# Optimization experiments

Hardware: AMD Instinct MI355X
Metric: run time of the kernel (lower is better)

## Reference

```python
import jax, jax.numpy as jnp
import numpy as np
import itertools

# ---- static config (mirrors args in init_kwargs) ----
BS = 4                        # num_processes
H, W = 480, 640               # frame_height, frame_width
NC = 16                       # num_sem_categories
C = 4 + NC                    # obs channels: RGB + depth + semantics
RES = 5                       # map_resolution (cm per cell)
ZRES = 5
MAP_CM = 4800 // 2            # map_size_cm // global_downscaling
M = MAP_CM // RES             # 480 local-map cells
VR = 100                      # vision_range
FOV = 79.0                    # hfov (deg)
DU = 1                        # du_scale
AGENT_H = 1.55 * 100.0        # camera_height * 100 (cm)
MAXH = int(360 / ZRES)        # 72
MINH = int(-40 / ZRES)        # -8
ZH = MAXH - MINH              # 80 height bins
MAP_THR, EXP_THR, CAT_THR = 1.0, 1.0, 5.0
DEG = 57.29577951308232
MIN_Z = int(5 / ZRES - MINH)                    # 9
MAX_Z = int((AGENT_H + 1 + 50) / ZRES - MINH)   # 49
XCAM = (W - 1.0) / 2.0
ZCAM = (H - 1.0) / 2.0
FOC = (W / 2.0) / np.tan(np.deg2rad(FOV / 2.0))


def _splat_feat_nd(feat, coords, grid_dims):
    # feat: (B,F,N) ; coords: (B,3,N) normalized to [-1,1] ; trilinear scatter-add
    B, Fc, N = feat.shape
    G = grid_dims[0] * grid_dims[1] * grid_dims[2]
    grid_flat = jnp.zeros((B, Fc, G), feat.dtype)
    pos_dim, wts_dim = [], []
    for d in range(3):
        gd = grid_dims[d]
        pos = coords[:, d, :] * (gd / 2.0) + gd / 2.0   # (B,N) voxel-space coord
        fl = jnp.floor(pos)
        pd, wd = [], []
        for ix in (0.0, 1.0):
            pos_ix = fl + ix
            safe = ((pos_ix > 0) & (pos_ix < gd)).astype(feat.dtype)
            wd.append((1.0 - jnp.abs(pos - pos_ix)) * safe)
            pd.append(pos_ix * safe)  # unsafe points dumped at index 0 with weight 0
        pos_dim.append(pd)
        wts_dim.append(wd)
    for ix_d in itertools.product((0, 1), (0, 1), (0, 1)):
        w = wts_dim[0][ix_d[0]] * wts_dim[1][ix_d[1]] * wts_dim[2][ix_d[2]]
        idx = jnp.zeros_like(w)
        for d in range(3):
            idx = idx * grid_dims[d] + pos_dim[d][ix_d[d]]
        idx = idx.astype(jnp.int32)                     # (B,N)
        vals = feat * w[:, None, :]                     # (B,F,N)
        grid_flat = jax.vmap(lambda g, i, v: g.at[:, i].add(v))(grid_flat, idx, vals)
    grid_flat = jnp.round(grid_flat)
    return grid_flat.reshape((B, Fc) + tuple(grid_dims))


def _affine_grid(theta, Hh, Ww):
    # align_corners=True base grid
    xs = jnp.linspace(-1.0, 1.0, Ww)
    ys = jnp.linspace(-1.0, 1.0, Hh)
    Xg, Yg = jnp.meshgrid(xs, ys)
    base = jnp.stack([Xg, Yg, jnp.ones_like(Xg)], -1)   # (H,W,3)
    return jnp.einsum('bij,hwj->bhwi', theta, base)     # (B,H,W,2)


def _grid_sample(img, grid):
    # bilinear, align_corners=True, zero padding; img (B,C,H,W), grid (B,Ho,Wo,2)
    B, Cc, Hh, Ww = img.shape
    x = (grid[..., 0] + 1.0) * 0.5 * (Ww - 1)
    y = (grid[..., 1] + 1.0) * 0.5 * (Hh - 1)
    x0 = jnp.floor(x)
    y0 = jnp.floor(y)
    wx1 = x - x0
    wy1 = y - y0

    def gather(ix, iy):
        valid = ((ix >= 0) & (ix <= Ww - 1) & (iy >= 0) & (iy <= Hh - 1)).astype(img.dtype)
        ixc = jnp.clip(ix, 0, Ww - 1).astype(jnp.int32)
        iyc = jnp.clip(iy, 0, Hh - 1).astype(jnp.int32)
        v = jax.vmap(lambda im, yy, xx: im[:, yy, xx])(img, iyc, ixc)  # (B,C,Ho,Wo)
        return v * valid[:, None]

    return (gather(x0, y0) * ((1 - wx1) * (1 - wy1))[:, None]
            + gather(x0 + 1, y0) * (wx1 * (1 - wy1))[:, None]
            + gather(x0, y0 + 1) * ((1 - wx1) * wy1)[:, None]
            + gather(x0 + 1, y0 + 1) * (wx1 * wy1)[:, None])


def _forward(obs, pose_obs, maps_last, poses_last, view_angles):
    bs = obs.shape[0]
    depth = obs[:, 3, ::DU, ::DU]                        # (B,h,w) depth in cm
    gx = jnp.arange(W, dtype=obs.dtype)[None, None, ::DU]
    gz = jnp.arange(H - 1, -1, -1, dtype=obs.dtype)[None, ::DU, None]
    Xp = (gx - XCAM) * depth / FOC
    Zp = (gz - ZCAM) * depth / FOC
    # rotate about x-axis by per-env view angle (deg), then lift by agent height
    a = jnp.deg2rad(view_angles)[:, None, None]
    ca, sa = jnp.cos(a), jnp.sin(a)
    Xv = Xp
    Yv = ca * depth - sa * Zp
    Zv = sa * depth + ca * Zp + AGENT_H
    # shift_loc rotation angle is pi/2 - pi/2 = 0 -> identity rot, only x shift
    Xv = Xv + VR * RES / 2.0
    # normalize to [-1,1] voxel coords
    xs = (Xv / RES - VR // 2.0) / VR * 2.0
    ys = (Yv / RES - VR // 2.0) / VR * 2.0
    zs = (Zv / ZRES - (MAXH + MINH) // 2.0) / (MAXH - MINH) * 2.0
    coords = jnp.stack([xs, ys, zs], 1).reshape(bs, 3, -1)   # (B,3,N)
    # features: channel 0 = ones (occupancy), rest = avg-pooled semantic masks
    sem = obs[:, 4:]
    pooled = sem.reshape(bs, NC, H // DU, DU, W // DU, DU).mean((3, 5))
    N = (H // DU) * (W // DU)
    feat = jnp.concatenate([jnp.ones((bs, 1, N), obs.dtype), pooled.reshape(bs, NC, N)], 1)
    voxels = _splat_feat_nd(feat, coords, (VR, VR, ZH)).swapaxes(2, 3)  # (B,1+NC,VR,VR,ZH)
    agg = voxels[..., MIN_Z:MAX_Z].sum(4)
    fp_map_pred = jnp.clip(agg[:, :1] / MAP_THR, 0.0, 1.0)
    fp_exp_pred = jnp.clip(voxels.sum(4)[:, :1] / EXP_THR, 0.0, 1.0)
    cat_pred = jnp.clip(agg[:, 1:] / CAT_THR, 0.0, 1.0)
    agent_view = jnp.zeros((bs, C, M, M), obs.dtype)
    x1 = M // 2 - VR // 2
    x2 = x1 + VR
    y1 = M // 2
    y2 = y1 + VR
    agent_view = agent_view.at[:, 0:1, y1:y2, x1:x2].set(fp_map_pred)
    agent_view = agent_view.at[:, 1:2, y1:y2, x1:x2].set(fp_exp_pred)
    agent_view = agent_view.at[:, 4:, y1:y2, x1:x2].set(cat_pred)
    # pose integration (get_new_pose_batch, note sequential in-place semantics)
    o = poses_last[:, 2] / DEG
    yy = poses_last[:, 1] + pose_obs[:, 0] * jnp.sin(o) + pose_obs[:, 1] * jnp.cos(o)
    xx = poses_last[:, 0] + pose_obs[:, 0] * jnp.cos(o) - pose_obs[:, 1] * jnp.sin(o)
    tt = poses_last[:, 2] + pose_obs[:, 2] * DEG
    tt = jnp.fmod(tt - 180.0, 360.0) + 180.0
    tt = jnp.fmod(tt + 180.0, 360.0) - 180.0
    current_poses = jnp.stack([xx, yy, tt], 1)
    # st_pose is detached in the original
    st = jax.lax.stop_gradient(current_poses)
    half = M // 2
    stx = -(st[:, 0] * 100.0 / RES - half) / half
    sty = -(st[:, 1] * 100.0 / RES - half) / half
    t = (90.0 - st[:, 2]) * np.pi / 180.0
    ct, s_t = jnp.cos(t), jnp.sin(t)
    zero, one = jnp.zeros_like(ct), jnp.ones_like(ct)
    theta1 = jnp.stack([jnp.stack([ct, -s_t, zero], 1), jnp.stack([s_t, ct, zero], 1)], 1)
    theta2 = jnp.stack([jnp.stack([one, zero, stx], 1), jnp.stack([zero, one, sty], 1)], 1)
    rotated = _grid_sample(agent_view, _affine_grid(theta1, M, M))
    translated = _grid_sample(rotated, _affine_grid(theta2, M, M))
    map_pred = jnp.maximum(maps_last, translated)
    # pose_pred aliases the in-place-updated poses_last in torch == current_poses
    return fp_map_pred, map_pred, current_poses, current_poses, translated


def setup_inputs() -> dict:
    key = jax.random.key(0)
    k1, k2, k3, k4 = jax.random.split(key, 4)
    obs = jax.random.uniform(k1, (BS, C, H, W), jnp.float32)
    obs = obs.at[:, 3].multiply(400.0)  # depth channel in cm, up to 4 m
    pose_obs = jax.random.uniform(k2, (BS, 3), jnp.float32) * 0.25
    maps_last = jax.random.uniform(k3, (BS, C, M, M), jnp.float32)
    poses_last = jax.random.uniform(k4, (BS, 3), jnp.float32)
    view_angles = jnp.zeros((BS,), jnp.float32)
    return {"obs": obs, "pose_obs": pose_obs, "maps_last": maps_last,
            "poses_last": poses_last, "view_angles": view_angles}


def reference(obs, pose_obs, maps_last, poses_last, view_angles):
    return _forward(obs, pose_obs, maps_last, poses_last, view_angles)
```

## Files before the change

kernel.cpp:

```cpp
#include <hip/hip_runtime.h>
#include <math.h>

#define BS 4
#define HH 480
#define WW 640
#define NPX (HH * WW)
#define NC 16
#define CHN 20
#define MM 480
#define VRD 100
#define ZHD 80
#define MINZ 9
#define MAXZ 49
#define CAP 4288
#define SLOTS (400 * CAP)

#define OFF0 0
#define OFF1 40000
#define OFF2 18472000
#define OFF3 18472012
#define OFF4 18472024
#define OFFSEM 40000
#define OFFGEO (OFFSEM + 16 * SLOTS)
#define OFFRB  (OFFGEO + 3 * SLOTS)
#define OFFMAP (OFFRB + 2 * SLOTS)
#define OFFCNT (OFFMAP + 720000)

__device__ __forceinline__ void pix2pos(int w, int h, float depth, float ca, float sa,
                                        float foc, float& px, float& py, float& pz) {
    float gx = (float)w;
    float gz = (float)(HH - 1 - h);
    float Xp = (gx - 319.5f) * depth / foc;
    float Zp = (gz - 239.5f) * depth / foc;
    float Yv = ca * depth - sa * Zp;
    float Zv = sa * depth + ca * Zp + 155.0f;
    float Xv = Xp + 250.0f;
    float xs = (Xv / 5.0f - 50.0f) / 100.0f * 2.0f;
    float ys = (Yv / 5.0f - 50.0f) / 100.0f * 2.0f;
    float zs = (Zv / 5.0f - 32.0f) / 80.0f * 2.0f;
    px = xs * 50.0f + 50.0f;
    py = ys * 50.0f + 50.0f;
    pz = zs * 40.0f + 40.0f;
}

__global__ __launch_bounds__(256) void bin_kernel(const float* __restrict__ obs,
                                                  const float* __restrict__ va,
                                                  int* __restrict__ cntA,
                                                  int* __restrict__ cntB,
                                                  float* __restrict__ gpx,
                                                  float* __restrict__ gpy,
                                                  float* __restrict__ gpz,
                                                  float* __restrict__ sem,
                                                  float2* __restrict__ recB,
                                                  float foc) {
    int idx = blockIdx.x * blockDim.x + threadIdx.x;
    if (idx >= BS * NPX) return;
    int b   = idx / NPX;
    int rem = idx % NPX;
    float depth = obs[((size_t)b * CHN + 3) * NPX + rem];
    int h = rem / WW, w = rem % WW;
    float a  = va[b] * 0.017453292519943295f;
    float ca = cosf(a), sa = sinf(a);
    float px, py, pz;
    pix2pos(w, h, depth, ca, sa, foc, px, py, pz);
    float ff = floorf(py);
    if (!(ff >= 0.0f && ff < 100.0f)) return;
    float fx = floorf(px);
    if (!(fx + 1.0f > 0.0f && fx < 100.0f)) return;
    int f = (int)ff;
    bool aok = (pz >= 8.0f && pz < 49.0f);
    bool bok = !aok && (pz >= 0.0f && pz < 80.0f);
    if (aok) {
        int slot = atomicAdd(cntA + (b * VRD + f) * 16, 1);
        if (slot < CAP) {
            int o = (b * VRD + f) * CAP + slot;
            gpx[o] = px; gpy[o] = py; gpz[o] = pz;
            const float* sp = obs + ((size_t)b * CHN + 4) * NPX + rem;
            #pragma unroll
            for (int c = 0; c < NC; c++) sem[(size_t)c * SLOTS + o] = sp[(size_t)c * NPX];
        }
    } else if (bok) {
        int slot = atomicAdd(cntB + (b * VRD + f) * 16, 1);
        if (slot < CAP) {
            float2 r; r.x = __int_as_float(rem); r.y = depth;
            recB[(b * VRD + f) * CAP + slot] = r;
        }
    }
}

__global__ __launch_bounds__(256, 5) void slice_kernel(const int* __restrict__ cntA,
                                                       const int* __restrict__ cntB,
                                                       const float* __restrict__ gpx,
                                                       const float* __restrict__ gpy,
                                                       const float* __restrict__ gpz,
                                                       const float* __restrict__ sem,
                                                       const float2* __restrict__ recB,
                                                       const float* __restrict__ va,
                                                       float* __restrict__ maps,
                                                       float* __restrict__ out0,
                                                       float foc) {
    __shared__ float acc[8000];
    int bid  = blockIdx.x;
    int wgid = (bid & 7) * 450 + (bid >> 3);
    int b  = wgid / 900;
    int r_ = wgid % 900;
    int g  = r_ / 100;
    int s  = r_ % 100;
    int tid = threadIdx.x;
    for (int i = tid; i < 8000; i += 256) acc[i] = 0.0f;
    __syncthreads();

    if (s > 0) {
        float fs = (float)s;
        int f0 = s - 1, f1 = s;
        int a0 = min(cntA[(b * VRD + f0) * 16], CAP);
        int a1 = min(cntA[(b * VRD + f1) * 16], CAP);
        int base0 = (b * VRD + f0) * CAP;
        int base1 = (b * VRD + f1) * CAP;
        int NA = a0 + a1;

        if (g < 8) {
            const float* s0p = sem + (size_t)(2 * g) * SLOTS;
            const float* s1p = sem + (size_t)(2 * g + 1) * SLOTS;
            for (int base = tid; base < NA; base += 1024) {
                int o[4]; bool vld[4];
                #pragma unroll
                for (int j = 0; j < 4; j++) {
                    int t = base + (j << 8);
                    vld[j] = (t < NA);
                    int oo = (t < a0) ? (base0 + t) : (base1 + (t - a0));
                    o[j] = vld[j] ? oo : base0;
                }
                float px[4], py[4], pz[4], v0[4], v1[4];
                #pragma unroll
                for (int j = 0; j < 4; j++) {
                    px[j] = gpx[o[j]]; py[j] = gpy[o[j]]; pz[j] = gpz[o[j]];
                    v0[j] = s0p[o[j]]; v1[j] = s1p[o[j]];
                }
                #pragma unroll
                for (int j = 0; j < 4; j++) {
                    if (!vld[j]) continue;
                    float wy = 1.0f - fabsf(py[j] - fs);
                    if (wy <= 0.0f) continue;
                    float fx = floorf(px[j]), fz = floorf(pz[j]);
                    #pragma unroll
                    for (int i2 = 0; i2 < 2; i2++) {
                        float cxp = fx + (float)i2;
                        if (!(cxp > 0.0f && cxp < 100.0f)) continue;
                        float wxy = wy * (1.0f - fabsf(px[j] - cxp));
                        int xi = (int)cxp;
                        #pragma unroll
                        for (int k = 0; k < 2; k++) {
                            float czp = fz + (float)k;
                            if (czp < 9.0f || czp >= 49.0f) continue;
                            float w3 = wxy * (1.0f - fabsf(pz[j] - czp));
                            if (w3 == 0.0f) continue;
                            float* dst = &acc[(((int)czp - MINZ) * VRD + xi) * 2];
                            atomicAdd(dst + 0, w3 * v0[j]);
                            atomicAdd(dst + 1, w3 * v1[j]);
                        }
                    }
                }
            }
        } else {
            for (int base = tid; base < NA; base += 1024) {
                int o[4]; bool vld[4];
                #pragma unroll
                for (int j = 0; j < 4; j++) {
                    int t = base + (j << 8);
                    vld[j] = (t < NA);
                    int oo = (t < a0) ? (base0 + t) : (base1 + (t - a0));
                    o[j] = vld[j] ? oo : base0;
                }
                float px[4], py[4], pz[4];
                #pragma unroll
                for (int j = 0; j < 4; j++) {
                    px[j] = gpx[o[j]]; py[j] = gpy[o[j]]; pz[j] = gpz[o[j]];
                }
                #pragma unroll
                for (int j = 0; j < 4; j++) {
                    if (!vld[j]) continue;
                    float wy = 1.0f - fabsf(py[j] - fs);
                    if (wy <= 0.0f) continue;
                    float fx = floorf(px[j]), fz = floorf(pz[j]);
                    #pragma unroll
                    for (int i2 = 0; i2 < 2; i2++) {
                        float cxp = fx + (float)i2;
                        if (!(cxp > 0.0f && cxp < 100.0f)) continue;
                        float wxy = wy * (1.0f - fabsf(px[j] - cxp));
                        int xi = (int)cxp;
                        #pragma unroll
                        for (int k = 0; k < 2; k++) {
                            float czp = fz + (float)k;
                            if (czp < 1.0f || czp >= 80.0f) continue;
                            float w3 = wxy * (1.0f - fabsf(pz[j] - czp));
                            if (w3 == 0.0f) continue;
                            atomicAdd(&acc[(int)czp * VRD + xi], w3);
                        }
                    }
                }
            }
            float a_  = va[b] * 0.017453292519943295f;
            float ca = cosf(a_), sa = sinf(a_);
            int b0 = min(cntB[(b * VRD + f0) * 16], CAP);
            int b1 = min(cntB[(b * VRD + f1) * 16], CAP);
            int NB = b0 + b1;
            for (int base = tid; base < NB; base += 1024) {
                float2 rv[4]; bool vld[4];
                #pragma unroll
                for (int j = 0; j < 4; j++) {
                    int t = base + (j << 8);
                    vld[j] = (t < NB);
                    int oo = (t < b0) ? (base0 + t) : (base1 + (t - b0));
                    rv[j] = vld[j] ? recB[oo] : make_float2(0.0f, 0.0f);
                }
                #pragma unroll
                for (int j = 0; j < 4; j++) {
                    if (!vld[j]) continue;
                    int rm = __float_as_int(rv[j].x);
                    float px, py, pz;
                    pix2pos(rm % WW, rm / WW, rv[j].y, ca, sa, foc, px, py, pz);
                    float wy = 1.0f - fabsf(py - fs);
                    if (wy <= 0.0f) continue;
                    float fx = floorf(px), fz = floorf(pz);
                    #pragma unroll
                    for (int i2 = 0; i2 < 2; i2++) {
                        float cxp = fx + (float)i2;
                        if (!(cxp > 0.0f && cxp < 100.0f)) continue;
                        float wxy = wy * (1.0f - fabsf(px - cxp));
                        int xi = (int)cxp;
                        #pragma unroll
                        for (int k = 0; k < 2; k++) {
                            float czp = fz + (float)k;
                            if (czp < 1.0f || czp >= 80.0f) continue;
                            float w3 = wxy * (1.0f - fabsf(pz - czp));
                            if (w3 == 0.0f) continue;
                            atomicAdd(&acc[(int)czp * VRD + xi], w3);
                        }
                    }
                }
            }
        }
    }
    __syncthreads();

    if (g < 8) {
        for (int i = tid; i < VRD * 2; i += 256) {
            int x = i >> 1, c = i & 1;
            float ssum = 0.0f;
            #pragma unroll 8
            for (int z = 0; z < 40; z++) ssum += rintf(acc[(z * VRD + x) * 2 + c]);
            maps[((size_t)(b * 18 + 2 + 2 * g + c) * VRD + s) * VRD + x] =
                fminf(fmaxf(ssum * 0.2f, 0.0f), 1.0f);
        }
    } else {
        for (int x = tid; x < VRD; x += 256) {
            float s_all = 0.0f, s_agg = 0.0f;
            #pragma unroll 8
            for (int z = 0; z < ZHD; z++) {
                float r = rintf(acc[z * VRD + x]);
                s_all += r;
                if (z >= MINZ && z < MAXZ) s_agg += r;
            }
            float fm = fminf(fmaxf(s_agg, 0.0f), 1.0f);
            float fe = fminf(fmaxf(s_all, 0.0f), 1.0f);
            maps[((size_t)(b * 18 + 0) * VRD + s) * VRD + x] = fm;
            maps[((size_t)(b * 18 + 1) * VRD + s) * VRD + x] = fe;
            out0[((size_t)b * VRD + s) * VRD + x] = fm;
        }
    }
}

__device__ __forceinline__ void pose_params(const float* __restrict__ pose_obs,
                                            const float* __restrict__ poses_last,
                                            int b, float& ct, float& st,
                                            float& stx, float& sty) {
    const float DEG = 57.29577951308232f;
    float o  = poses_last[b*3+2] / DEG;
    float so = sinf(o), co = cosf(o);
    float yy = poses_last[b*3+1] + pose_obs[b*3+0]*so + pose_obs[b*3+1]*co;
    float xx = poses_last[b*3+0] + pose_obs[b*3+0]*co - pose_obs[b*3+1]*so;
    float tt = poses_last[b*3+2] + pose_obs[b*3+2]*DEG;
    tt = fmodf(tt - 180.0f, 360.0f) + 180.0f;
    tt = fmodf(tt + 180.0f, 360.0f) - 180.0f;
    stx = -((xx*100.0f/5.0f) - 240.0f) / 240.0f;
    sty = -((yy*100.0f/5.0f) - 240.0f) / 240.0f;
    float t = (90.0f - tt) * 0.017453292519943295f;
    ct = cosf(t); st = sinf(t);
}

__global__ __launch_bounds__(64) void pose_kernel(const float* __restrict__ pose_obs,
                                                  const float* __restrict__ poses_last,
                                                  float* __restrict__ out) {
    int b = threadIdx.x;
    if (b >= BS) return;
    const float DEG = 57.29577951308232f;
    float o  = poses_last[b*3+2] / DEG;
    float so = sinf(o), co = cosf(o);
    float yy = poses_last[b*3+1] + pose_obs[b*3+0]*so + pose_obs[b*3+1]*co;
    float xx = poses_last[b*3+0] + pose_obs[b*3+0]*co - pose_obs[b*3+1]*so;
    float tt = poses_last[b*3+2] + pose_obs[b*3+2]*DEG;
    tt = fmodf(tt - 180.0f, 360.0f) + 180.0f;
    tt = fmodf(tt + 180.0f, 360.0f) - 180.0f;
    out[OFF2 + b*3+0] = xx; out[OFF2 + b*3+1] = yy; out[OFF2 + b*3+2] = tt;
    out[OFF3 + b*3+0] = xx; out[OFF3 + b*3+1] = yy; out[OFF3 + b*3+2] = tt;
}

__global__ __launch_bounds__(256) void rotate_kernel(const float* __restrict__ maps,
                                                     const float* __restrict__ pose_obs,
                                                     const float* __restrict__ poses_last,
                                                     float* __restrict__ rot) {
    int idx = blockIdx.x * blockDim.x + threadIdx.x;
    if (idx >= BS * MM * MM) return;
    int b   = idx / (MM * MM);
    int rem = idx % (MM * MM);
    int y   = rem / MM;
    int x   = rem % MM;
    float ct, st, stx, sty;
    pose_params(pose_obs, poses_last, b, ct, st, stx, sty);
    float Xg = -1.0f + (float)x * (2.0f / 479.0f);
    float Yg = -1.0f + (float)y * (2.0f / 479.0f);
    float gx = ct * Xg - st * Yg;
    float gy = st * Xg + ct * Yg;
    float xf = (gx + 1.0f) * 0.5f * 479.0f;
    float yf = (gy + 1.0f) * 0.5f * 479.0f;
    float x0 = floorf(xf), y0 = floorf(yf);
    float fx = xf - x0, fy = yf - y0;
    float cw[4] = {(1.0f - fx) * (1.0f - fy), fx * (1.0f - fy),
                   (1.0f - fx) * fy,          fx * fy};
    float cx[4] = {x0, x0 + 1.0f, x0, x0 + 1.0f};
    float cy[4] = {y0, y0, y0 + 1.0f, y0 + 1.0f};
    float acc[18];
    #pragma unroll
    for (int m = 0; m < 18; m++) acc[m] = 0.0f;
    #pragma unroll
    for (int k = 0; k < 4; k++) {
        float fxk = cx[k], fyk = cy[k];
        if (!(fxk >= 0.0f && fxk <= 479.0f && fyk >= 0.0f && fyk <= 479.0f)) continue;
        int ix = (int)fxk, iy = (int)fyk;
        if (iy < 240 || iy >= 340 || ix < 190 || ix >= 290) continue;
        int mi = iy - 240, mj = ix - 190;
        float w = cw[k];
        const float* mp = maps + (size_t)b * 18 * VRD * VRD + mi * VRD + mj;
        #pragma unroll
        for (int m = 0; m < 18; m++) acc[m] += w * mp[(size_t)m * VRD * VRD];
    }
    size_t obase = ((size_t)b * CHN) * MM * MM + (size_t)y * MM + x;
    rot[obase + (size_t)0 * MM * MM] = acc[0];
    rot[obase + (size_t)1 * MM * MM] = acc[1];
    rot[obase + (size_t)2 * MM * MM] = 0.0f;
    rot[obase + (size_t)3 * MM * MM] = 0.0f;
    #pragma unroll
    for (int m = 2; m < 18; m++)
        rot[obase + (size_t)(m + 2) * MM * MM] = acc[m];
}

__global__ __launch_bounds__(256) void translate_kernel(const float* __restrict__ rot,
                                                        const float* __restrict__ pose_obs,
                                                        const float* __restrict__ poses_last,
                                                        float* __restrict__ tr) {
    int idx = blockIdx.x * blockDim.x + threadIdx.x;
    if (idx >= BS * MM * MM) return;
    int b   = idx / (MM * MM);
    int rem = idx % (MM * MM);
    int y   = rem / MM;
    int x   = rem % MM;
    float ct, st, stx, sty;
    pose_params(pose_obs, poses_last, b, ct, st, stx, sty);
    float Xg = -1.0f + (float)x * (2.0f / 479.0f);
    float Yg = -1.0f + (float)y * (2.0f / 479.0f);
    float xf = (Xg + stx + 1.0f) * 0.5f * 479.0f;
    float yf = (Yg + sty + 1.0f) * 0.5f * 479.0f;
    float x0 = floorf(xf), y0 = floorf(yf);
    float fx = xf - x0, fy = yf - y0;
    float cw[4] = {(1.0f - fx) * (1.0f - fy), fx * (1.0f - fy),
                   (1.0f - fx) * fy,          fx * fy};
    float cxs[4] = {x0, x0 + 1.0f, x0, x0 + 1.0f};
    float cys[4] = {y0, y0, y0 + 1.0f, y0 + 1.0f};
    bool vk[4]; int offk[4];
    #pragma unroll
    for (int k = 0; k < 4; k++) {
        vk[k] = (cxs[k] >= 0.0f && cxs[k] <= 479.0f && cys[k] >= 0.0f && cys[k] <= 479.0f);
        offk[k] = vk[k] ? ((int)cys[k] * MM + (int)cxs[k]) : 0;
    }
    #pragma unroll
    for (int c = 0; c < CHN; c++) {
        const float* rp = rot + ((size_t)b * CHN + c) * MM * MM;
        float v = 0.0f;
        #pragma unroll
        for (int k = 0; k < 4; k++)
            if (vk[k]) v += cw[k] * rp[offk[k]];
        tr[((size_t)b * CHN + c) * MM * MM + (size_t)y * MM + x] = v;
    }
}

__global__ __launch_bounds__(256) void max_kernel(const float* __restrict__ maps_last,
                                                  const float* __restrict__ tr,
                                                  float* __restrict__ mp) {
    int i = blockIdx.x * blockDim.x + threadIdx.x;
    int n4 = BS * CHN * MM * MM / 4;
    if (i >= n4) return;
    float4 a = ((const float4*)maps_last)[i];
    float4 t = ((const float4*)tr)[i];
    float4 r;
    r.x = fmaxf(a.x, t.x);
    r.y = fmaxf(a.y, t.y);
    r.z = fmaxf(a.z, t.z);
    r.w = fmaxf(a.w, t.w);
    ((float4*)mp)[i] = r;
}

extern "C" void kernel_launch(void* const* d_in, const int* in_sizes, int n_in,
                              void* d_out, int out_size, void* d_ws, size_t ws_size,
                              hipStream_t stream) {
    const float* obs         = (const float*)d_in[0];
    const float* pose_obs    = (const float*)d_in[1];
    const float* maps_last   = (const float*)d_in[2];
    const float* poses_last  = (const float*)d_in[3];
    const float* view_angles = (const float*)d_in[4];
    float* out = (float*)d_out;

    float*  sem   = out + OFFSEM;
    float*  gpx   = out + OFFGEO;
    float*  gpy   = out + OFFGEO + SLOTS;
    float*  gpz   = out + OFFGEO + 2 * SLOTS;
    float2* recB  = (float2*)(out + OFFRB);
    float*  maps  = out + OFFMAP;
    int*    cntA  = (int*)(out + OFFCNT);
    int*    cntB  = cntA + 6400;

    hipMemsetAsync(cntA, 0, 12800 * sizeof(int), stream);

    const float foc = (float)(320.0 / tan(39.5 * M_PI / 180.0));

    int npix = BS * NPX;
    bin_kernel<<<(npix + 255) / 256, 256, 0, stream>>>(obs, view_angles, cntA, cntB,
                                                       gpx, gpy, gpz, sem, recB, foc);

    slice_kernel<<<dim3(VRD * BS * 9), 256, 0, stream>>>(cntA, cntB, gpx, gpy, gpz,
                                                         sem, recB, view_angles,
                                                         maps, out + OFF0, foc);

    pose_kernel<<<1, 64, 0, stream>>>(pose_obs, poses_last, out);

    int nmap = BS * MM * MM;
    rotate_kernel<<<(nmap + 255) / 256, 256, 0, stream>>>(maps, pose_obs, poses_last,
                                                          out + OFF1);
    translate_kernel<<<(nmap + 255) / 256, 256, 0, stream>>>(out + OFF1, pose_obs,
                                                             poses_last, out + OFF4);
    int n4 = BS * CHN * MM * MM / 4;
    max_kernel<<<(n4 + 255) / 256, 256, 0, stream>>>(maps_last, out + OFF4, out + OFF1);
}
```

Measured before the change: 1.385 ms.

## Coalesce per-thread splat runs into register accumulators before shared atomics

Each thread now handles a contiguous chunk of the point list instead of a strided set, and keeps four corner accumulators in registers keyed by the base voxel. It flushes to the shared-memory histogram only when the voxel changes. The aim is to cut LDS atomic traffic and contention when neighbouring points fall in the same voxel. In exchange, global loads lose coalescing because adjacent threads read distant addresses, there is less memory-level parallelism from dropping the 4-way unroll, and summation order changes slightly.

```diff
diff --git a/kernel.cpp b/kernel.cpp
--- a/kernel.cpp
+++ b/kernel.cpp
@@ -122,123 +122,126 @@
         if (g < 8) {
             const float* s0p = sem + (size_t)(2 * g) * SLOTS;
             const float* s1p = sem + (size_t)(2 * g + 1) * SLOTS;
-            for (int base = tid; base < NA; base += 1024) {
-                int o[4]; bool vld[4];
-                #pragma unroll
-                for (int j = 0; j < 4; j++) {
-                    int t = base + (j << 8);
-                    vld[j] = (t < NA);
-                    int oo = (t < a0) ? (base0 + t) : (base1 + (t - a0));
-                    o[j] = vld[j] ? oo : base0;
+            int chunk = (NA + 255) >> 8;
+            int beg = tid * chunk;
+            int end = min(beg + chunk, NA);
+            int key = -1;
+            float a00c0 = 0, a00c1 = 0, a01c0 = 0, a01c1 = 0;
+            float a10c0 = 0, a10c1 = 0, a11c0 = 0, a11c1 = 0;
+            auto flushS = [&]() {
+                if (key < 0) return;
+                int ix = key >> 7, iz = key & 127;
+                bool vx0 = ix > 0, vx1 = ix < 99;
+                bool vz0 = iz >= 9, vz1 = iz <= 47;
+                if (vx0 && vz0) { float* d = &acc[((iz - 9) * VRD + ix) * 2];
+                                  atomicAdd(d, a00c0); atomicAdd(d + 1, a00c1); }
+                if (vx0 && vz1) { float* d = &acc[((iz - 8) * VRD + ix) * 2];
+                                  atomicAdd(d, a01c0); atomicAdd(d + 1, a01c1); }
+                if (vx1 && vz0) { float* d = &acc[((iz - 9) * VRD + ix + 1) * 2];
+                                  atomicAdd(d, a10c0); atomicAdd(d + 1, a10c1); }
+                if (vx1 && vz1) { float* d = &acc[((iz - 8) * VRD + ix + 1) * 2];
+                                  atomicAdd(d, a11c0); atomicAdd(d + 1, a11c1); }
+            };
+            for (int t = beg; t < end; t++) {
+                int o = (t < a0) ? (base0 + t) : (base1 + (t - a0));
+                float px = gpx[o], py = gpy[o], pz = gpz[o];
+                float wy = 1.0f - fabsf(py - fs);
+                if (wy <= 0.0f) continue;
+                float fx = floorf(px), fz = floorf(pz);
+                int k2 = ((int)fx << 7) | (int)fz;
+                if (k2 != key) {
+                    flushS();
+                    key = k2;
+                    a00c0 = a00c1 = a01c0 = a01c1 = 0.0f;
+                    a10c0 = a10c1 = a11c0 = a11c1 = 0.0f;
                 }
-                float px[4], py[4], pz[4], v0[4], v1[4];
-                #pragma unroll
-                for (int j = 0; j < 4; j++) {
-                    px[j] = gpx[o[j]]; py[j] = gpy[o[j]]; pz[j] = gpz[o[j]];
-                    v0[j] = s0p[o[j]]; v1[j] = s1p[o[j]];
-                }
-                #pragma unroll
-                for (int j = 0; j < 4; j++) {
-                    if (!vld[j]) continue;
-                    float wy = 1.0f - fabsf(py[j] - fs);
-                    if (wy <= 0.0f) continue;
-                    float fx = floorf(px[j]), fz = floorf(pz[j]);
-                    #pragma unroll
-                    for (int i2 = 0; i2 < 2; i2++) {
-                        float cxp = fx + (float)i2;
-                        if (!(cxp > 0.0f && cxp < 100.0f)) continue;
-                        float wxy = wy * (1.0f - fabsf(px[j] - cxp));
-                        int xi = (int)cxp;
-                        #pragma unroll
-                        for (int k = 0; k < 2; k++) {
-                            float czp = fz + (float)k;
-                            if (czp < 9.0f || czp >= 49.0f) continue;
-                            float w3 = wxy * (1.0f - fabsf(pz[j] - czp));
-                            if (w3 == 0.0f) continue;
-                            float* dst = &acc[(((int)czp - MINZ) * VRD + xi) * 2];
-                            atomicAdd(dst + 0, w3 * v0[j]);
-                            atomicAdd(dst + 1, w3 * v1[j]);
-                        }
-                    }
-                }
+                float v0 = s0p[o], v1 = s1p[o];
+                float wx0 = 1.0f - fabsf(px - fx);
+                float wx1 = 1.0f - fabsf(px - (fx + 1.0f));
+                float wz0 = 1.0f - fabsf(pz - fz);
+                float wz1 = 1.0f - fabsf(pz - (fz + 1.0f));
+                float wxy0 = wy * wx0, wxy1 = wy * wx1;
+                float w00 = wxy0 * wz0, w01 = wxy0 * wz1;
+                float w10 = wxy1 * wz0, w11 = wxy1 * wz1;
+                a00c0 += w00 * v0; a00c1 += w00 * v1;
+                a01c0 += w01 * v0; a01c1 += w01 * v1;
+                a10c0 += w10 * v0; a10c1 += w10 * v1;
+                a11c0 += w11 * v0; a11c1 += w11 * v1;
             }
+            flushS();
         } else {
-            for (int base = tid; base < NA; base += 1024) {
-                int o[4]; bool vld[4];
-                #pragma unroll
-                for (int j = 0; j < 4; j++) {
-                    int t = base + (j << 8);
-                    vld[j] = (t < NA);
-                    int oo = (t < a0) ? (base0 + t) : (base1 + (t - a0));
-                    o[j] = vld[j] ? oo : base0;
-                }
-                float px[4], py[4], pz[4];
-                #pragma unroll
-                for (int j = 0; j < 4; j++) {
-                    px[j] = gpx[o[j]]; py[j] = gpy[o[j]]; pz[j] = gpz[o[j]];
-                }
-                #pragma unroll
-                for (int j = 0; j < 4; j++) {
-                    if (!vld[j]) continue;
-                    float wy = 1.0f - fabsf(py[j] - fs);
-                    if (wy <= 0.0f) continue;
-                    float fx = floorf(px[j]), fz = floorf(pz[j]);
-                    #pragma unroll
-                    for (int i2 = 0; i2 < 2; i2++) {
-                        float cxp = fx + (float)i2;
-                        if (!(cxp > 0.0f && cxp < 100.0f)) continue;
-                        float wxy = wy * (1.0f - fabsf(px[j] - cxp));
-                        int xi = (int)cxp;
-                        #pragma unroll
-                        for (int k = 0; k < 2; k++) {
-                            float czp = fz + (float)k;
-                            if (czp < 1.0f || czp >= 80.0f) continue;
-                            float w3 = wxy * (1.0f - fabsf(pz[j] - czp));
-                            if (w3 == 0.0f) continue;
-                            atomicAdd(&acc[(int)czp * VRD + xi], w3);
-                        }
-                    }
-                }
-            }
-            float a_  = va[b] * 0.017453292519943295f;
-            float ca = cosf(a_), sa = sinf(a_);
-            int b0 = min(cntB[(b * VRD + f0) * 16], CAP);
-            int b1 = min(cntB[(b * VRD + f1) * 16], CAP);
-            int NB = b0 + b1;
-            for (int base = tid; base < NB; base += 1024) {
-                float2 rv[4]; bool vld[4];
-                #pragma unroll
-                for (int j = 0; j < 4; j++) {
-                    int t = base + (j << 8);
-                    vld[j] = (t < NB);
-                    int oo = (t < b0) ? (base0 + t) : (base1 + (t - b0));
-                    rv[j] = vld[j] ? recB[oo] : make_float2(0.0f, 0.0f);
-                }
-                #pragma unroll
-                for (int j = 0; j < 4; j++) {
-                    if (!vld[j]) continue;
-                    int rm = __float_as_int(rv[j].x);
-                    float px, py, pz;
-                    pix2pos(rm % WW, rm / WW, rv[j].y, ca, sa, foc, px, py, pz);
+            int key = -1;
+            float a00 = 0, a01 = 0, a10 = 0, a11 = 0;
+            auto flushO = [&]() {
+                if (key < 0) return;
+                int ix = key >> 7, iz = key & 127;
+                bool vx0 = ix > 0, vx1 = ix < 99;
+                bool vz0 = iz >= 1, vz1 = iz <= 78;
+                if (vx0 && vz0) atomicAdd(&acc[iz * VRD + ix], a00);
+                if (vx0 && vz1) atomicAdd(&acc[(iz + 1) * VRD + ix], a01);
+                if (vx1 && vz0) atomicAdd(&acc[iz * VRD + ix + 1], a10);
+                if (vx1 && vz1) atomicAdd(&acc[(iz + 1) * VRD + ix + 1], a11);
+            };
+            {
+                int chunk = (NA + 255) >> 8;
+                int beg = tid * chunk;
+                int end = min(beg + chunk, NA);
+                for (int t = beg; t < end; t++) {
+                    int o = (t < a0) ? (base0 + t) : (base1 + (t - a0));
+                    float px = gpx[o], py = gpy[o], pz = gpz[o];
                     float wy = 1.0f - fabsf(py - fs);
                     if (wy <= 0.0f) continue;
                     float fx = floorf(px), fz = floorf(pz);
-                    #pragma unroll
-                    for (int i2 = 0; i2 < 2; i2++) {
-                        float cxp = fx + (float)i2;
-                        if (!(cxp > 0.0f && cxp < 100.0f)) continue;
-                        float wxy = wy * (1.0f - fabsf(px - cxp));
-                        int xi = (int)cxp;
-                        #pragma unroll
-                        for (int k = 0; k < 2; k++) {
-                            float czp = fz + (float)k;
-                            if (czp < 1.0f || czp >= 80.0f) continue;
-                            float w3 = wxy * (1.0f - fabsf(pz - czp));
-                            if (w3 == 0.0f) continue;
-                            atomicAdd(&acc[(int)czp * VRD + xi], w3);
-                        }
+                    int k2 = ((int)fx << 7) | (int)fz;
+                    if (k2 != key) {
+                        flushO();
+                        key = k2;
+                        a00 = a01 = a10 = a11 = 0.0f;
                     }
+                    float wx0 = 1.0f - fabsf(px - fx);
+                    float wx1 = 1.0f - fabsf(px - (fx + 1.0f));
+                    float wz0 = 1.0f - fabsf(pz - fz);
+                    float wz1 = 1.0f - fabsf(pz - (fz + 1.0f));
+                    float wxy0 = wy * wx0, wxy1 = wy * wx1;
+                    a00 += wxy0 * wz0; a01 += wxy0 * wz1;
+                    a10 += wxy1 * wz0; a11 += wxy1 * wz1;
                 }
+                flushO();
+                key = -1; a00 = a01 = a10 = a11 = 0.0f;
+            }
+            {
+                float a_ = va[b] * 0.017453292519943295f;
+                float ca = cosf(a_), sa = sinf(a_);
+                int b0 = min(cntB[(b * VRD + f0) * 16], CAP);
+                int b1 = min(cntB[(b * VRD + f1) * 16], CAP);
+                int NB = b0 + b1;
+                int chunk = (NB + 255) >> 8;
+                int beg = tid * chunk;
+                int end = min(beg + chunk, NB);
+                for (int t = beg; t < end; t++) {
+                    int o = (t < b0) ? (base0 + t) : (base1 + (t - b0));
+                    float2 rv = recB[o];
+                    int rm = __float_as_int(rv.x);
+                    float px, py, pz;
+                    pix2pos(rm % WW, rm / WW, rv.y, ca, sa, foc, px, py, pz);
+                    float wy = 1.0f - fabsf(py - fs);
+                    if (wy <= 0.0f) continue;
+                    float fx = floorf(px), fz = floorf(pz);
+                    int k2 = ((int)fx << 7) | (int)fz;
+                    if (k2 != key) {
+                        flushO();
+                        key = k2;
+                        a00 = a01 = a10 = a11 = 0.0f;
+                    }
+                    float wx0 = 1.0f - fabsf(px - fx);
+                    float wx1 = 1.0f - fabsf(px - (fx + 1.0f));
+                    float wz0 = 1.0f - fabsf(pz - fz);
+                    float wz1 = 1.0f - fabsf(pz - (fz + 1.0f));
+                    float wxy0 = wy * wx0, wxy1 = wy * wx1;
+                    a00 += wxy0 * wz0; a01 += wxy0 * wz1;
+                    a10 += wxy1 * wz0; a11 += wxy1 * wz1;
+                }
+                flushO();
             }
         }
     }
```

Measured after the change: 1.341 ms. -3.2%, faster.
